# Kernel optimization log

Hardware: AMD Instinct MI355X
Metric: run time of the kernel (lower is better)

The kernel has to match this reference:

```python
import jax, jax.numpy as jnp
import numpy as np

D = 256        # n_unit
H = 2          # n_head
FF = 256       # n_hid
WIN = 99       # N-1 in source: row i attends to cols [i-99, i]
NEG = -1e30    # additive mask value (-inf in torch)
LN_EPS = 1e-5


def _layer_norm(x, w, b):
    mu = jnp.mean(x, axis=-1, keepdims=True)
    var = jnp.mean((x - mu) ** 2, axis=-1, keepdims=True)
    return (x - mu) * jax.lax.rsqrt(var + LN_EPS) * w + b


def _pos_encoding(S, d):
    pos = jnp.arange(S, dtype=jnp.float32)[:, None]                      # [S,1]
    div = jnp.exp(jnp.arange(0, d, 2, dtype=jnp.float32) * (-np.log(10000.0) / d))
    ang = pos * div                                                      # [S,d/2]
    return jnp.stack([jnp.sin(ang), jnp.cos(ang)], axis=-1).reshape(S, d)


def _band_mask(S):
    i = jnp.arange(S)[:, None]
    j = jnp.arange(S)[None, :]
    allowed = (j <= i) & (j >= i - WIN)
    return jnp.where(allowed, 0.0, NEG).astype(jnp.float32)             # [S,S]


def setup_inputs() -> dict:
    key = jax.random.key(0)
    ks = jax.random.split(key, 24)
    B, S, IN = 8, 2000, 256
    s = 0.02
    inp = {
        "src": jax.random.normal(ks[0], (B, S, IN), jnp.float32),
        "input_lengths": jax.random.randint(ks[1], (B,), 1, S + 1).astype(jnp.int64),
        # encoder Linear(in_size, n_unit); torch Linear weight is [out,in]
        "W_enc": jax.random.normal(ks[2], (D, IN), jnp.float32) * s,
        "b_enc": jnp.zeros((D,), jnp.float32),
        # MHA packed qkv projection
        "in_proj_w": jax.random.normal(ks[3], (3 * D, D), jnp.float32) * s,
        "in_proj_b": jnp.zeros((3 * D,), jnp.float32),
        "out_proj_w": jax.random.normal(ks[4], (D, D), jnp.float32) * s,
        "out_proj_b": jnp.zeros((D,), jnp.float32),
        "ln1_w": jnp.ones((D,), jnp.float32),
        "ln1_b": jnp.zeros((D,), jnp.float32),
        # FFN
        "lin1_w": jax.random.normal(ks[5], (FF, D), jnp.float32) * s,
        "lin1_b": jnp.zeros((FF,), jnp.float32),
        "lin2_w": jax.random.normal(ks[6], (D, FF), jnp.float32) * s,
        "lin2_b": jnp.zeros((D,), jnp.float32),
        "ln2_w": jnp.ones((D,), jnp.float32),
        "ln2_b": jnp.zeros((D,), jnp.float32),
        # output head
        "fc1_w": jax.random.normal(ks[7], (D // 4, D), jnp.float32) * s,
        "fc1_b": jnp.zeros((D // 4,), jnp.float32),
        "fc2_w": jax.random.normal(ks[8], (1, D // 4), jnp.float32) * s,
        "fc2_b": jnp.zeros((1,), jnp.float32),
    }
    return inp


def reference(src, input_lengths, W_enc, b_enc, in_proj_w, in_proj_b,
              out_proj_w, out_proj_b, ln1_w, ln1_b, lin1_w, lin1_b,
              lin2_w, lin2_b, ln2_w, ln2_b, fc1_w, fc1_b, fc2_w, fc2_b):
    B, S, _ = src.shape
    hd = D // H
    # input projection + positional encoding (dropout is identity at eval)
    x = src @ W_enc.T + b_enc                                            # [B,S,D]
    x = x + _pos_encoding(S, D)[None]
    # --- TransformerEncoderLayer (post-norm, relu) with banded causal mask ---
    qkv = x @ in_proj_w.T + in_proj_b                                    # [B,S,3D]
    q, k, v = jnp.split(qkv, 3, axis=-1)
    q = q.reshape(B, S, H, hd)
    k = k.reshape(B, S, H, hd)
    v = v.reshape(B, S, H, hd)
    scores = jnp.einsum('bihd,bjhd->bhij', q, k) / np.sqrt(hd)           # [B,H,S,S]
    scores = scores + _band_mask(S)[None, None]
    attn = jax.nn.softmax(scores, axis=-1)
    ctx = jnp.einsum('bhij,bjhd->bihd', attn, v).reshape(B, S, D)
    attn_out = ctx @ out_proj_w.T + out_proj_b
    x = _layer_norm(x + attn_out, ln1_w, ln1_b)
    ff = jax.nn.relu(x @ lin1_w.T + lin1_b) @ lin2_w.T + lin2_b
    x = _layer_norm(x + ff, ln2_w, ln2_b)
    # --- output head (no activation between fc1 and fc2, per source) ---
    out = x @ fc1_w.T + fc1_b                                            # [B,S,D/4]
    logits = out @ fc2_w.T + fc2_b                                       # [B,S,1]
    return logits.reshape(B, -1)                                         # [B,S]
```

## Files before the change

### kernel.cpp

```cpp
#include <hip/hip_runtime.h>
#include <math.h>

#define SLEN 2000
#define BATCH 8
#define MTOK 16000
#define WIN 99
#define XPAD 264

typedef __attribute__((ext_vector_type(8))) short short8;
typedef __attribute__((ext_vector_type(4))) float floatx4;

__device__ __forceinline__ float bf2f(unsigned int h) {
  union { unsigned int u; float f; } w; w.u = h << 16; return w.f;
}
__device__ __forceinline__ unsigned short f2bf(float f) {
  union { float f; unsigned int u; } w; w.f = f;
  return (unsigned short)((w.u + 0x7fffu + ((w.u >> 16) & 1u)) >> 16);
}

__device__ __forceinline__ void cvt4(const float* __restrict__ in,
                                     unsigned short* __restrict__ out, int i) {
  float4 v = ((const float4*)in)[i];
  ushort4 o;
  o.x = f2bf(v.x); o.y = f2bf(v.y); o.z = f2bf(v.z); o.w = f2bf(v.w);
  ((ushort4*)out)[i] = o;
}

__global__ __launch_bounds__(256) void k_prep(
    const float* __restrict__ wenc,     unsigned short* __restrict__ wencb,
    const float* __restrict__ wqk,      unsigned short* __restrict__ wqkb,
    const float* __restrict__ wout,     unsigned short* __restrict__ woutb,
    const float* __restrict__ wl1,      unsigned short* __restrict__ wl1b,
    const float* __restrict__ wl2,      unsigned short* __restrict__ wl2b,
    float* __restrict__ pe,
    const float* __restrict__ fc1w, const float* __restrict__ fc1b,
    const float* __restrict__ fc2w, const float* __restrict__ fc2b,
    const float* __restrict__ ln2w, const float* __restrict__ ln2b,
    float* __restrict__ hp) {
  __shared__ float red0[4], red1[4];
  const int bx = blockIdx.x, tid = threadIdx.x;
  if (bx < 64)         { cvt4(wenc, wencb, bx * 256 + tid); }
  else if (bx < 256)   { cvt4(wqk,  wqkb,  (bx - 64) * 256 + tid); }
  else if (bx < 320)   { cvt4(wout, woutb, (bx - 256) * 256 + tid); }
  else if (bx < 384)   { cvt4(wl1,  wl1b,  (bx - 320) * 256 + tid); }
  else if (bx < 448)   { cvt4(wl2,  wl2b,  (bx - 384) * 256 + tid); }
  else if (bx < 948) {
    int i4 = (bx - 448) * 256 + tid;
    int e0 = i4 * 4;
    int s  = e0 >> 8;
    int d0 = e0 & 255;
    float dv0 = expf((float)(d0 >> 1) * -0.07195578415606394f);
    float dv1 = expf((float)((d0 >> 1) + 1) * -0.07195578415606394f);
    float a0 = (float)s * dv0, a1 = (float)s * dv1;
    ((float4*)pe)[i4] = make_float4(sinf(a0), cosf(a0), sinf(a1), cosf(a1));
  } else {
    int k = tid;
    float we = 0.f;
#pragma unroll 8
    for (int o = 0; o < 64; ++o) we += fc2w[o] * fc1w[o * 256 + k];
    float c1 = ln2w[k] * we;
    hp[k] = c1;
    float p0 = ln2b[k] * we;
    if (k < 64) p0 += fc2w[k] * fc1b[k];
    float s0 = p0, s1 = c1;
#pragma unroll
    for (int off = 32; off; off >>= 1) {
      s0 += __shfl_xor(s0, off);
      s1 += __shfl_xor(s1, off);
    }
    int wv = k >> 6;
    if ((k & 63) == 0) { red0[wv] = s0; red1[wv] = s1; }
    __syncthreads();
    if (k == 0) {
      hp[256] = red0[0] + red0[1] + red0[2] + red0[3] + fc2b[0];
      hp[257] = red1[0] + red1[1] + red1[2] + red1[3];
    }
  }
}

__global__ __launch_bounds__(512) void k_pre(
    const float* __restrict__ src,
    const unsigned short* __restrict__ wenc, const float* __restrict__ benc,
    const float* __restrict__ pe,
    const unsigned short* __restrict__ wqk, const float* __restrict__ bqk,
    unsigned short* __restrict__ xb, unsigned short* __restrict__ qkvb) {
  __shared__ __align__(16) unsigned short Xt[64 * XPAD];
  const int tid = threadIdx.x, lane = tid & 63, w = tid >> 6;
  const int m0 = blockIdx.x * 64;
  const int kq = lane >> 4, ml = lane & 15;

  {
    const int cb = w * 32;
    floatx4 acc[4][2] = {};
#pragma unroll
    for (int k8 = 0; k8 < 8; ++k8) {
      const int kt = k8 * 32;
      short8 af[4];
#pragma unroll
      for (int mt = 0; mt < 4; ++mt) {
        const float* ap = src + (size_t)(m0 + mt * 16 + ml) * 256 + kt + kq * 8;
        float4 v0 = *(const float4*)ap;
        float4 v1 = *(const float4*)(ap + 4);
        unsigned short t8[8] = {f2bf(v0.x), f2bf(v0.y), f2bf(v0.z), f2bf(v0.w),
                                f2bf(v1.x), f2bf(v1.y), f2bf(v1.z), f2bf(v1.w)};
        af[mt] = *(const short8*)t8;
      }
#pragma unroll
      for (int nt = 0; nt < 2; ++nt) {
        short8 bf = *(const short8*)(wenc + (size_t)(cb + nt * 16 + ml) * 256 + kt + kq * 8);
#pragma unroll
        for (int mt = 0; mt < 4; ++mt)
          acc[mt][nt] = __builtin_amdgcn_mfma_f32_16x16x32_bf16(af[mt], bf, acc[mt][nt], 0, 0, 0);
      }
    }
#pragma unroll
    for (int mt = 0; mt < 4; ++mt)
#pragma unroll
      for (int nt = 0; nt < 2; ++nt)
#pragma unroll
        for (int r = 0; r < 4; ++r) {
          int lrow = mt * 16 + kq * 4 + r;
          int col  = cb + nt * 16 + ml;
          float v = acc[mt][nt][r] + benc[col]
                  + pe[(size_t)((m0 + lrow) % SLEN) * 256 + col];
          unsigned short hv = f2bf(v);
          Xt[lrow * XPAD + col] = hv;
          xb[(size_t)(m0 + lrow) * 256 + col] = hv;
        }
  }
  __syncthreads();

  {
    const int cb = w * 96;
    floatx4 acc[4][6] = {};
#pragma unroll
    for (int k8 = 0; k8 < 8; ++k8) {
      const int kt = k8 * 32;
      short8 af[4];
#pragma unroll
      for (int mt = 0; mt < 4; ++mt)
        af[mt] = *(const short8*)&Xt[(mt * 16 + ml) * XPAD + kt + kq * 8];
#pragma unroll
      for (int nt = 0; nt < 6; ++nt) {
        short8 bf = *(const short8*)(wqk + (size_t)(cb + nt * 16 + ml) * 256 + kt + kq * 8);
#pragma unroll
        for (int mt = 0; mt < 4; ++mt)
          acc[mt][nt] = __builtin_amdgcn_mfma_f32_16x16x32_bf16(af[mt], bf, acc[mt][nt], 0, 0, 0);
      }
    }
#pragma unroll
    for (int mt = 0; mt < 4; ++mt)
#pragma unroll
      for (int nt = 0; nt < 6; ++nt)
#pragma unroll
        for (int r = 0; r < 4; ++r) {
          int row = m0 + mt * 16 + kq * 4 + r;
          int cg  = cb + nt * 16 + ml;
          qkvb[(size_t)row * 768 + cg] = f2bf(acc[mt][nt][r] + bqk[cg]);
        }
  }
}

#define KPAD 136
#define VPAD 184
#define PPAD 132
#define UNION 176

__global__ __launch_bounds__(256) void k_attn_mfma(const unsigned short* __restrict__ qkv,
                                                   unsigned short* __restrict__ ctx) {
  __shared__ __align__(16) unsigned short KV[UNION * KPAD];
  __shared__ __align__(16) unsigned short Ps[4][16 * PPAD];
  const int tid  = threadIdx.x;
  const int lane = tid & 63;
  const int w    = tid >> 6;
  const int i0   = blockIdx.x * 64;
  const int b    = blockIdx.y;
  const int h    = blockIdx.z;
  const int jmin_u = i0 - WIN;
  const float scale = 0.08838834764831845f;

  const int qrow = i0 + w * 16 + (lane & 15);
  const unsigned short* qptr =
      qkv + (size_t)(b * SLEN + min(qrow, SLEN - 1)) * 768 + h * 128 + (lane >> 4) * 8;
  short8 qf[4];
#pragma unroll
  for (int kc = 0; kc < 4; ++kc) qf[kc] = *(const short8*)(qptr + kc * 32);

  for (int it = 0; it < 11; ++it) {
    int idx = it * 256 + tid;
    int row = idx >> 4;
    int c8  = idx & 15;
    int j = jmin_u + row;
    uint4 v = make_uint4(0u, 0u, 0u, 0u);
    if (j >= 0 && j < SLEN)
      v = *(const uint4*)(qkv + (size_t)(b * SLEN + j) * 768 + 256 + h * 128 + c8 * 8);
    *(uint4*)&KV[row * KPAD + c8 * 8] = v;
  }
  __syncthreads();

  const int koff = w * 16;
  floatx4 sc[8] = {};
#pragma unroll
  for (int kt = 0; kt < 8; ++kt) {
#pragma unroll
    for (int kc = 0; kc < 4; ++kc) {
      short8 kf = *(const short8*)&KV[(koff + kt * 16 + (lane & 15)) * KPAD
                                      + kc * 32 + (lane >> 4) * 8];
      sc[kt] = __builtin_amdgcn_mfma_f32_16x16x32_bf16(qf[kc], kf, sc[kt], 0, 0, 0);
    }
  }

  const int qme = i0 + w * 16 + (lane >> 4) * 4;
  const int jme = jmin_u + koff + (lane & 15);
  float mx[4] = {-1e30f, -1e30f, -1e30f, -1e30f};
#pragma unroll
  for (int kt = 0; kt < 8; ++kt) {
#pragma unroll
    for (int r = 0; r < 4; ++r) {
      int j = jme + kt * 16, q = qme + r;
      bool ok = (j >= 0) && (j >= q - WIN) && (j <= q);
      float s = ok ? sc[kt][r] : -1e30f;
      sc[kt][r] = s;
      mx[r] = fmaxf(mx[r], s);
    }
  }
#pragma unroll
  for (int r = 0; r < 4; ++r)
#pragma unroll
    for (int off = 8; off; off >>= 1) mx[r] = fmaxf(mx[r], __shfl_xor(mx[r], off, 16));

  float sum[4] = {0.f, 0.f, 0.f, 0.f};
#pragma unroll
  for (int kt = 0; kt < 8; ++kt)
#pragma unroll
    for (int r = 0; r < 4; ++r) {
      float e = __expf((sc[kt][r] - mx[r]) * scale);
      sc[kt][r] = e;
      sum[r] += e;
    }
#pragma unroll
  for (int r = 0; r < 4; ++r)
#pragma unroll
    for (int off = 8; off; off >>= 1) sum[r] += __shfl_xor(sum[r], off, 16);
  float rinv[4];
#pragma unroll
  for (int r = 0; r < 4; ++r) rinv[r] = 1.f / sum[r];

  unsigned short* pw = &Ps[w][0];
#pragma unroll
  for (int kt = 0; kt < 8; ++kt)
#pragma unroll
    for (int r = 0; r < 4; ++r)
      pw[((lane >> 4) * 4 + r) * PPAD + kt * 16 + (lane & 15)] = f2bf(sc[kt][r]);
  __syncthreads();

  for (int it = 0; it < 12; ++it) {
    int idx = it * 256 + tid;
    int grp = idx >> 6;
    int key = (grp >> 4) * 64 + (idx & 63);
    int c8  = grp & 15;
    if (key < UNION) {
      int j = jmin_u + key;
      uint4 v = make_uint4(0u, 0u, 0u, 0u);
      if (j >= 0 && j < SLEN)
        v = *(const uint4*)(qkv + (size_t)(b * SLEN + j) * 768 + 512 + h * 128 + c8 * 8);
      unsigned short e[8];
      *(uint4*)e = v;
      int d0 = c8 * 8;
#pragma unroll
      for (int i = 0; i < 8; ++i) KV[(d0 + i) * VPAD + key] = e[i];
    }
  }
  __syncthreads();

  floatx4 ov[8] = {};
#pragma unroll
  for (int kc = 0; kc < 4; ++kc) {
    short8 pf = *(const short8*)&pw[(lane & 15) * PPAD + kc * 32 + (lane >> 4) * 8];
#pragma unroll
    for (int dt = 0; dt < 8; ++dt) {
      short8 vf = *(const short8*)&KV[(dt * 16 + (lane & 15)) * VPAD
                                      + koff + kc * 32 + (lane >> 4) * 8];
      ov[dt] = __builtin_amdgcn_mfma_f32_16x16x32_bf16(pf, vf, ov[dt], 0, 0, 0);
    }
  }

#pragma unroll
  for (int dt = 0; dt < 8; ++dt)
#pragma unroll
    for (int r = 0; r < 4; ++r) {
      int q = qme + r;
      if (q < SLEN)
        ctx[(size_t)(b * SLEN + q) * 256 + h * 128 + dt * 16 + (lane & 15)] =
            f2bf(ov[dt][r] * rinv[r]);
    }
}

__global__ __launch_bounds__(512) void k_post(
    const unsigned short* __restrict__ ctx,
    const unsigned short* __restrict__ wout, const float* __restrict__ bout,
    const unsigned short* __restrict__ xb,
    const float* __restrict__ ln1w, const float* __restrict__ ln1b,
    const unsigned short* __restrict__ w1, const float* __restrict__ b1,
    const unsigned short* __restrict__ w2, const float* __restrict__ b2,
    const float* __restrict__ hp, float* __restrict__ out) {
  __shared__ __align__(16) unsigned short X1[64 * XPAD];
  __shared__ float lnred[8][64][3];
  __shared__ float lnstat[64][2];
  __shared__ float lnp[512];
  __shared__ float c1s[256];
  const int tid = threadIdx.x, lane = tid & 63, w = tid >> 6;
  const int m0 = blockIdx.x * 64;
  const int kq = lane >> 4, ml = lane & 15;
  const int cb = w * 32;

  if (tid < 256) {
    lnp[tid] = ln1w[tid];
    lnp[256 + tid] = ln1b[tid];
    c1s[tid] = hp[tid];
  }
  const float c0h = hp[256], sc1 = hp[257];

  floatx4 acc[4][2] = {};
#pragma unroll
  for (int k8 = 0; k8 < 8; ++k8) {
    const int kt = k8 * 32;
    short8 af[4];
#pragma unroll
    for (int mt = 0; mt < 4; ++mt)
      af[mt] = *(const short8*)(ctx + (size_t)(m0 + mt * 16 + ml) * 256 + kt + kq * 8);
#pragma unroll
    for (int nt = 0; nt < 2; ++nt) {
      short8 bf = *(const short8*)(wout + (size_t)(cb + nt * 16 + ml) * 256 + kt + kq * 8);
#pragma unroll
      for (int mt = 0; mt < 4; ++mt)
        acc[mt][nt] = __builtin_amdgcn_mfma_f32_16x16x32_bf16(af[mt], bf, acc[mt][nt], 0, 0, 0);
    }
  }
  float s_[4][4], q_[4][4];
#pragma unroll
  for (int mt = 0; mt < 4; ++mt)
#pragma unroll
    for (int r = 0; r < 4; ++r) { s_[mt][r] = 0.f; q_[mt][r] = 0.f; }
#pragma unroll
  for (int mt = 0; mt < 4; ++mt)
#pragma unroll
    for (int nt = 0; nt < 2; ++nt)
#pragma unroll
      for (int r = 0; r < 4; ++r) {
        int lrow = mt * 16 + kq * 4 + r;
        int col  = cb + nt * 16 + ml;
        float v = acc[mt][nt][r] + bout[col]
                + bf2f(xb[(size_t)(m0 + lrow) * 256 + col]);
        acc[mt][nt][r] = v;
        s_[mt][r] += v;
        q_[mt][r] += v * v;
      }
#pragma unroll
  for (int mt = 0; mt < 4; ++mt)
#pragma unroll
    for (int r = 0; r < 4; ++r) {
#pragma unroll
      for (int off = 8; off; off >>= 1) {
        s_[mt][r] += __shfl_xor(s_[mt][r], off, 16);
        q_[mt][r] += __shfl_xor(q_[mt][r], off, 16);
      }
      if (ml == 0) {
        int lrow = mt * 16 + kq * 4 + r;
        lnred[w][lrow][0] = s_[mt][r];
        lnred[w][lrow][1] = q_[mt][r];
      }
    }
  __syncthreads();
  if (tid < 64) {
    float s = 0.f, q = 0.f;
#pragma unroll
    for (int i = 0; i < 8; ++i) { s += lnred[i][tid][0]; q += lnred[i][tid][1]; }
    float mu  = s * (1.f / 256.f);
    float var = q * (1.f / 256.f) - mu * mu;
    lnstat[tid][0] = mu;
    lnstat[tid][1] = rsqrtf(var + 1e-5f);
  }
  __syncthreads();
  floatx4 x1sav[4][2];
#pragma unroll
  for (int mt = 0; mt < 4; ++mt)
#pragma unroll
    for (int r = 0; r < 4; ++r) {
      int lrow = mt * 16 + kq * 4 + r;
      float mu = lnstat[lrow][0], rr = lnstat[lrow][1];
#pragma unroll
      for (int nt = 0; nt < 2; ++nt) {
        int col = cb + nt * 16 + ml;
        float x1 = (acc[mt][nt][r] - mu) * rr * lnp[col] + lnp[256 + col];
        x1sav[mt][nt][r] = x1;
        X1[lrow * XPAD + col] = f2bf(x1);
      }
    }
  __syncthreads();

#pragma unroll
  for (int mt = 0; mt < 4; ++mt)
#pragma unroll
    for (int nt = 0; nt < 2; ++nt) acc[mt][nt] = (floatx4){0.f, 0.f, 0.f, 0.f};
#pragma unroll
  for (int k8 = 0; k8 < 8; ++k8) {
    const int kt = k8 * 32;
    short8 af[4];
#pragma unroll
    for (int mt = 0; mt < 4; ++mt)
      af[mt] = *(const short8*)&X1[(mt * 16 + ml) * XPAD + kt + kq * 8];
#pragma unroll
    for (int nt = 0; nt < 2; ++nt) {
      short8 bf = *(const short8*)(w1 + (size_t)(cb + nt * 16 + ml) * 256 + kt + kq * 8);
#pragma unroll
      for (int mt = 0; mt < 4; ++mt)
        acc[mt][nt] = __builtin_amdgcn_mfma_f32_16x16x32_bf16(af[mt], bf, acc[mt][nt], 0, 0, 0);
    }
  }
  __syncthreads();
#pragma unroll
  for (int mt = 0; mt < 4; ++mt)
#pragma unroll
    for (int nt = 0; nt < 2; ++nt)
#pragma unroll
      for (int r = 0; r < 4; ++r) {
        int lrow = mt * 16 + kq * 4 + r;
        int col  = cb + nt * 16 + ml;
        X1[lrow * XPAD + col] = f2bf(fmaxf(acc[mt][nt][r] + b1[col], 0.f));
      }
  __syncthreads();

#pragma unroll
  for (int mt = 0; mt < 4; ++mt)
#pragma unroll
    for (int nt = 0; nt < 2; ++nt) acc[mt][nt] = (floatx4){0.f, 0.f, 0.f, 0.f};
#pragma unroll
  for (int k8 = 0; k8 < 8; ++k8) {
    const int kt = k8 * 32;
    short8 af[4];
#pragma unroll
    for (int mt = 0; mt < 4; ++mt)
      af[mt] = *(const short8*)&X1[(mt * 16 + ml) * XPAD + kt + kq * 8];
#pragma unroll
    for (int nt = 0; nt < 2; ++nt) {
      short8 bf = *(const short8*)(w2 + (size_t)(cb + nt * 16 + ml) * 256 + kt + kq * 8);
#pragma unroll
      for (int mt = 0; mt < 4; ++mt)
        acc[mt][nt] = __builtin_amdgcn_mfma_f32_16x16x32_bf16(af[mt], bf, acc[mt][nt], 0, 0, 0);
    }
  }
  float ss[4][4], qq[4][4], dd[4][4];
#pragma unroll
  for (int mt = 0; mt < 4; ++mt)
#pragma unroll
    for (int r = 0; r < 4; ++r) { ss[mt][r] = 0.f; qq[mt][r] = 0.f; dd[mt][r] = 0.f; }
#pragma unroll
  for (int mt = 0; mt < 4; ++mt)
#pragma unroll
    for (int nt = 0; nt < 2; ++nt)
#pragma unroll
      for (int r = 0; r < 4; ++r) {
        int col = cb + nt * 16 + ml;
        float v = acc[mt][nt][r] + b2[col] + x1sav[mt][nt][r];
        ss[mt][r] += v;
        qq[mt][r] += v * v;
        dd[mt][r] += v * c1s[col];
      }
#pragma unroll
  for (int mt = 0; mt < 4; ++mt)
#pragma unroll
    for (int r = 0; r < 4; ++r) {
#pragma unroll
      for (int off = 8; off; off >>= 1) {
        ss[mt][r] += __shfl_xor(ss[mt][r], off, 16);
        qq[mt][r] += __shfl_xor(qq[mt][r], off, 16);
        dd[mt][r] += __shfl_xor(dd[mt][r], off, 16);
      }
      if (ml == 0) {
        int lrow = mt * 16 + kq * 4 + r;
        lnred[w][lrow][0] = ss[mt][r];
        lnred[w][lrow][1] = qq[mt][r];
        lnred[w][lrow][2] = dd[mt][r];
      }
    }
  __syncthreads();
  if (tid < 64) {
    float s = 0.f, q = 0.f, d = 0.f;
#pragma unroll
    for (int i = 0; i < 8; ++i) {
      s += lnred[i][tid][0];
      q += lnred[i][tid][1];
      d += lnred[i][tid][2];
    }
    float mu  = s * (1.f / 256.f);
    float var = q * (1.f / 256.f) - mu * mu;
    float rr  = rsqrtf(var + 1e-5f);
    out[m0 + tid] = rr * (d - mu * sc1) + c0h;
  }
}

extern "C" void kernel_launch(void* const* d_in, const int* in_sizes, int n_in,
                              void* d_out, int out_size, void* d_ws, size_t ws_size,
                              hipStream_t stream) {
  const float* src        = (const float*)d_in[0];
  const float* W_enc      = (const float*)d_in[2];
  const float* b_enc      = (const float*)d_in[3];
  const float* in_proj_w  = (const float*)d_in[4];
  const float* in_proj_b  = (const float*)d_in[5];
  const float* out_proj_w = (const float*)d_in[6];
  const float* out_proj_b = (const float*)d_in[7];
  const float* ln1_w      = (const float*)d_in[8];
  const float* ln1_b      = (const float*)d_in[9];
  const float* lin1_w     = (const float*)d_in[10];
  const float* lin1_b     = (const float*)d_in[11];
  const float* lin2_w     = (const float*)d_in[12];
  const float* lin2_b     = (const float*)d_in[13];
  const float* ln2_w      = (const float*)d_in[14];
  const float* ln2_b      = (const float*)d_in[15];
  const float* fc1_w      = (const float*)d_in[16];
  const float* fc1_b      = (const float*)d_in[17];
  const float* fc2_w      = (const float*)d_in[18];
  const float* fc2_b      = (const float*)d_in[19];

  char* p = (char*)d_ws;
  float* pe            = (float*)p;           p += (size_t)SLEN * 256 * 4;
  float* hp            = (float*)p;           p += 2048;
  unsigned short* xb   = (unsigned short*)p;  p += (size_t)MTOK * 256 * 2;
  unsigned short* qkvb = (unsigned short*)p;  p += (size_t)MTOK * 768 * 2;
  unsigned short* ctxb = (unsigned short*)p;  p += (size_t)MTOK * 256 * 2;
  unsigned short* wencb= (unsigned short*)p;  p += 256 * 256 * 2;
  unsigned short* wqkb = (unsigned short*)p;  p += 768 * 256 * 2;
  unsigned short* woutb= (unsigned short*)p;  p += 256 * 256 * 2;
  unsigned short* wl1b = (unsigned short*)p;  p += 256 * 256 * 2;
  unsigned short* wl2b = (unsigned short*)p;  p += 256 * 256 * 2;

  k_prep<<<949, 256, 0, stream>>>(W_enc, wencb, in_proj_w, wqkb,
                                  out_proj_w, woutb, lin1_w, wl1b, lin2_w, wl2b,
                                  pe, fc1_w, fc1_b, fc2_w, fc2_b, ln2_w, ln2_b, hp);
  k_pre<<<MTOK / 64, 512, 0, stream>>>(src, wencb, b_enc, pe, wqkb, in_proj_b, xb, qkvb);
  k_attn_mfma<<<dim3((SLEN + 63) / 64, BATCH, 2), 256, 0, stream>>>(qkvb, ctxb);
  k_post<<<MTOK / 64, 512, 0, stream>>>(ctxb, woutb, out_proj_b, xb, ln1_w, ln1_b,
                                        wl1b, lin1_b, wl2b, lin2_b, hp, (float*)d_out);
}
```

Before: 188.8 us.

## Fuse attention with post-projection/FFN, drop prep kernel and compute posenc inline

Removes the separate weight-conversion/positional-encoding prep kernel. Weights are now converted fp32->bf16 on the fly inside the GEMM loops, and positional encoding is computed inline with fast sin. Attention for both heads is merged with the out-projection, LN, FFN and output head into a single kernel, so the ctx buffer round-trip through global memory disappears. Blocks change from 512 to 256 threads. The trade-offs are redundant weight conversion per block, fewer attention blocks (the head dimension moves into the loop), and heavier shared-memory use, which may lower occupancy.

New measurement: 235.1 us. 24.5% more time.

```diff
diff --git a/kernel.cpp b/kernel.cpp
--- a/kernel.cpp
+++ b/kernel.cpp
@@ -17,146 +17,92 @@
   union { float f; unsigned int u; } w; w.f = f;
   return (unsigned short)((w.u + 0x7fffu + ((w.u >> 16) & 1u)) >> 16);
 }
-
-__device__ __forceinline__ void cvt4(const float* __restrict__ in,
-                                     unsigned short* __restrict__ out, int i) {
-  float4 v = ((const float4*)in)[i];
-  ushort4 o;
-  o.x = f2bf(v.x); o.y = f2bf(v.y); o.z = f2bf(v.z); o.w = f2bf(v.w);
-  ((ushort4*)out)[i] = o;
-}
-
-__global__ __launch_bounds__(256) void k_prep(
-    const float* __restrict__ wenc,     unsigned short* __restrict__ wencb,
-    const float* __restrict__ wqk,      unsigned short* __restrict__ wqkb,
-    const float* __restrict__ wout,     unsigned short* __restrict__ woutb,
-    const float* __restrict__ wl1,      unsigned short* __restrict__ wl1b,
-    const float* __restrict__ wl2,      unsigned short* __restrict__ wl2b,
-    float* __restrict__ pe,
-    const float* __restrict__ fc1w, const float* __restrict__ fc1b,
-    const float* __restrict__ fc2w, const float* __restrict__ fc2b,
-    const float* __restrict__ ln2w, const float* __restrict__ ln2b,
-    float* __restrict__ hp) {
-  __shared__ float red0[4], red1[4];
-  const int bx = blockIdx.x, tid = threadIdx.x;
-  if (bx < 64)         { cvt4(wenc, wencb, bx * 256 + tid); }
-  else if (bx < 256)   { cvt4(wqk,  wqkb,  (bx - 64) * 256 + tid); }
-  else if (bx < 320)   { cvt4(wout, woutb, (bx - 256) * 256 + tid); }
-  else if (bx < 384)   { cvt4(wl1,  wl1b,  (bx - 320) * 256 + tid); }
-  else if (bx < 448)   { cvt4(wl2,  wl2b,  (bx - 384) * 256 + tid); }
-  else if (bx < 948) {
-    int i4 = (bx - 448) * 256 + tid;
-    int e0 = i4 * 4;
-    int s  = e0 >> 8;
-    int d0 = e0 & 255;
-    float dv0 = expf((float)(d0 >> 1) * -0.07195578415606394f);
-    float dv1 = expf((float)((d0 >> 1) + 1) * -0.07195578415606394f);
-    float a0 = (float)s * dv0, a1 = (float)s * dv1;
-    ((float4*)pe)[i4] = make_float4(sinf(a0), cosf(a0), sinf(a1), cosf(a1));
-  } else {
-    int k = tid;
-    float we = 0.f;
-#pragma unroll 8
-    for (int o = 0; o < 64; ++o) we += fc2w[o] * fc1w[o * 256 + k];
-    float c1 = ln2w[k] * we;
-    hp[k] = c1;
-    float p0 = ln2b[k] * we;
-    if (k < 64) p0 += fc2w[k] * fc1b[k];
-    float s0 = p0, s1 = c1;
-#pragma unroll
-    for (int off = 32; off; off >>= 1) {
-      s0 += __shfl_xor(s0, off);
-      s1 += __shfl_xor(s1, off);
-    }
-    int wv = k >> 6;
-    if ((k & 63) == 0) { red0[wv] = s0; red1[wv] = s1; }
-    __syncthreads();
-    if (k == 0) {
-      hp[256] = red0[0] + red0[1] + red0[2] + red0[3] + fc2b[0];
-      hp[257] = red1[0] + red1[1] + red1[2] + red1[3];
-    }
-  }
-}
-
-__global__ __launch_bounds__(512) void k_pre(
+__device__ __forceinline__ short8 cvt_row8(const float* __restrict__ p) {
+  float4 v0 = *(const float4*)p;
+  float4 v1 = *(const float4*)(p + 4);
+  unsigned short t8[8] = {f2bf(v0.x), f2bf(v0.y), f2bf(v0.z), f2bf(v0.w),
+                          f2bf(v1.x), f2bf(v1.y), f2bf(v1.z), f2bf(v1.w)};
+  return *(const short8*)t8;
+}
+__device__ __forceinline__ float posenc_val(int spos, int col) {
+  float p   = (float)(col >> 1);
+  float dv  = __expf(p * -0.07195578415606394f);
+  float ang = (float)spos * dv;
+  float rev = ang * 0.15915494309189535f;
+  rev -= floorf(rev);
+  if (col & 1) { rev += 0.25f; rev -= floorf(rev); }
+  return __sinf(rev * 6.283185307179586f);
+}
+
+__global__ __launch_bounds__(256) void k_pre(
     const float* __restrict__ src,
-    const unsigned short* __restrict__ wenc, const float* __restrict__ benc,
-    const float* __restrict__ pe,
-    const unsigned short* __restrict__ wqk, const float* __restrict__ bqk,
+    const float* __restrict__ wenc, const float* __restrict__ benc,
+    const float* __restrict__ wqk,  const float* __restrict__ bqk,
     unsigned short* __restrict__ xb, unsigned short* __restrict__ qkvb) {
   __shared__ __align__(16) unsigned short Xt[64 * XPAD];
   const int tid = threadIdx.x, lane = tid & 63, w = tid >> 6;
   const int m0 = blockIdx.x * 64;
   const int kq = lane >> 4, ml = lane & 15;
-
-  {
-    const int cb = w * 32;
-    floatx4 acc[4][2] = {};
+  const int wcol = w * 64;
+
+  floatx4 acc[4][4] = {};
+#pragma unroll
+  for (int k8 = 0; k8 < 8; ++k8) {
+    const int kt = k8 * 32;
+    short8 af[4];
+#pragma unroll
+    for (int mt = 0; mt < 4; ++mt)
+      af[mt] = cvt_row8(src + (size_t)(m0 + mt * 16 + ml) * 256 + kt + kq * 8);
+#pragma unroll
+    for (int nt = 0; nt < 4; ++nt) {
+      short8 bf = cvt_row8(wenc + (size_t)(wcol + nt * 16 + ml) * 256 + kt + kq * 8);
+#pragma unroll
+      for (int mt = 0; mt < 4; ++mt)
+        acc[mt][nt] = __builtin_amdgcn_mfma_f32_16x16x32_bf16(af[mt], bf, acc[mt][nt], 0, 0, 0);
+    }
+  }
+#pragma unroll
+  for (int mt = 0; mt < 4; ++mt)
+#pragma unroll
+    for (int nt = 0; nt < 4; ++nt)
+#pragma unroll
+      for (int r = 0; r < 4; ++r) {
+        int lrow = mt * 16 + kq * 4 + r;
+        int col  = wcol + nt * 16 + ml;
+        int spos = (m0 + lrow) % SLEN;
+        float v = acc[mt][nt][r] + benc[col] + posenc_val(spos, col);
+        unsigned short hv = f2bf(v);
+        Xt[lrow * XPAD + col] = hv;
+        xb[(size_t)(m0 + lrow) * 256 + col] = hv;
+      }
+  __syncthreads();
+
+  for (int p = 0; p < 3; ++p) {
+    floatx4 a2[4][4] = {};
 #pragma unroll
     for (int k8 = 0; k8 < 8; ++k8) {
       const int kt = k8 * 32;
       short8 af[4];
 #pragma unroll
-      for (int mt = 0; mt < 4; ++mt) {
-        const float* ap = src + (size_t)(m0 + mt * 16 + ml) * 256 + kt + kq * 8;
-        float4 v0 = *(const float4*)ap;
-        float4 v1 = *(const float4*)(ap + 4);
-        unsigned short t8[8] = {f2bf(v0.x), f2bf(v0.y), f2bf(v0.z), f2bf(v0.w),
-                                f2bf(v1.x), f2bf(v1.y), f2bf(v1.z), f2bf(v1.w)};
-        af[mt] = *(const short8*)t8;
-      }
-#pragma unroll
-      for (int nt = 0; nt < 2; ++nt) {
-        short8 bf = *(const short8*)(wenc + (size_t)(cb + nt * 16 + ml) * 256 + kt + kq * 8);
-#pragma unroll
-        for (int mt = 0; mt < 4; ++mt)
-          acc[mt][nt] = __builtin_amdgcn_mfma_f32_16x16x32_bf16(af[mt], bf, acc[mt][nt], 0, 0, 0);
-      }
-    }
-#pragma unroll
-    for (int mt = 0; mt < 4; ++mt)
-#pragma unroll
-      for (int nt = 0; nt < 2; ++nt)
-#pragma unroll
-        for (int r = 0; r < 4; ++r) {
-          int lrow = mt * 16 + kq * 4 + r;
-          int col  = cb + nt * 16 + ml;
-          float v = acc[mt][nt][r] + benc[col]
-                  + pe[(size_t)((m0 + lrow) % SLEN) * 256 + col];
-          unsigned short hv = f2bf(v);
-          Xt[lrow * XPAD + col] = hv;
-          xb[(size_t)(m0 + lrow) * 256 + col] = hv;
-        }
-  }
-  __syncthreads();
-
-  {
-    const int cb = w * 96;
-    floatx4 acc[4][6] = {};
-#pragma unroll
-    for (int k8 = 0; k8 < 8; ++k8) {
-      const int kt = k8 * 32;
-      short8 af[4];
-#pragma unroll
       for (int mt = 0; mt < 4; ++mt)
         af[mt] = *(const short8*)&Xt[(mt * 16 + ml) * XPAD + kt + kq * 8];
 #pragma unroll
-      for (int nt = 0; nt < 6; ++nt) {
-        short8 bf = *(const short8*)(wqk + (size_t)(cb + nt * 16 + ml) * 256 + kt + kq * 8);
+      for (int nt = 0; nt < 4; ++nt) {
+        short8 bf = cvt_row8(wqk + (size_t)(p * 256 + wcol + nt * 16 + ml) * 256 + kt + kq * 8);
 #pragma unroll
         for (int mt = 0; mt < 4; ++mt)
-          acc[mt][nt] = __builtin_amdgcn_mfma_f32_16x16x32_bf16(af[mt], bf, acc[mt][nt], 0, 0, 0);
+          a2[mt][nt] = __builtin_amdgcn_mfma_f32_16x16x32_bf16(af[mt], bf, a2[mt][nt], 0, 0, 0);
       }
     }
 #pragma unroll
     for (int mt = 0; mt < 4; ++mt)
 #pragma unroll
-      for (int nt = 0; nt < 6; ++nt)
+      for (int nt = 0; nt < 4; ++nt)
 #pragma unroll
         for (int r = 0; r < 4; ++r) {
           int row = m0 + mt * 16 + kq * 4 + r;
-          int cg  = cb + nt * 16 + ml;
-          qkvb[(size_t)row * 768 + cg] = f2bf(acc[mt][nt][r] + bqk[cg]);
+          int cg  = p * 256 + wcol + nt * 16 + ml;
+          qkvb[(size_t)row * 768 + cg] = f2bf(a2[mt][nt][r] + bqk[cg]);
         }
   }
 }
@@ -166,172 +112,188 @@
 #define PPAD 132
 #define UNION 176
 
-__global__ __launch_bounds__(256) void k_attn_mfma(const unsigned short* __restrict__ qkv,
-                                                   unsigned short* __restrict__ ctx) {
-  __shared__ __align__(16) unsigned short KV[UNION * KPAD];
-  __shared__ __align__(16) unsigned short Ps[4][16 * PPAD];
-  const int tid  = threadIdx.x;
-  const int lane = tid & 63;
-  const int w    = tid >> 6;
-  const int i0   = blockIdx.x * 64;
-  const int b    = blockIdx.y;
-  const int h    = blockIdx.z;
+__global__ __launch_bounds__(256) void k_ap(
+    const unsigned short* __restrict__ qkv,
+    const unsigned short* __restrict__ xb,
+    const float* __restrict__ wout, const float* __restrict__ bout,
+    const float* __restrict__ ln1w, const float* __restrict__ ln1b,
+    const float* __restrict__ w1,   const float* __restrict__ b1,
+    const float* __restrict__ w2,   const float* __restrict__ b2,
+    const float* __restrict__ fc1w, const float* __restrict__ fc1b,
+    const float* __restrict__ fc2w, const float* __restrict__ fc2b,
+    const float* __restrict__ ln2w, const float* __restrict__ ln2b,
+    float* __restrict__ out) {
+  __shared__ __align__(16) unsigned char smem[64768];
+  unsigned short* KV  = (unsigned short*)smem;
+  unsigned short* Ps  = (unsigned short*)(smem + 47872);
+  unsigned short* CX  = (unsigned short*)smem;
+  float* lnred  = (float*)(smem + 33792);
+  float* lnstat = (float*)(smem + 36864);
+  float* lnp    = (float*)(smem + 37376);
+  float* c1s    = (float*)(smem + 39424);
+  float* hpred  = (float*)(smem + 40448);
+  float* hpc    = (float*)(smem + 40480);
+
+  const int tid = threadIdx.x, lane = tid & 63, w = tid >> 6;
+  const int i0 = blockIdx.x * 64;
+  const int b  = blockIdx.y;
   const int jmin_u = i0 - WIN;
+  const int kq = lane >> 4, ml = lane & 15;
   const float scale = 0.08838834764831845f;
 
-  const int qrow = i0 + w * 16 + (lane & 15);
-  const unsigned short* qptr =
-      qkv + (size_t)(b * SLEN + min(qrow, SLEN - 1)) * 768 + h * 128 + (lane >> 4) * 8;
-  short8 qf[4];
-#pragma unroll
-  for (int kc = 0; kc < 4; ++kc) qf[kc] = *(const short8*)(qptr + kc * 32);
-
-  for (int it = 0; it < 11; ++it) {
-    int idx = it * 256 + tid;
-    int row = idx >> 4;
-    int c8  = idx & 15;
-    int j = jmin_u + row;
-    uint4 v = make_uint4(0u, 0u, 0u, 0u);
-    if (j >= 0 && j < SLEN)
-      v = *(const uint4*)(qkv + (size_t)(b * SLEN + j) * 768 + 256 + h * 128 + c8 * 8);
-    *(uint4*)&KV[row * KPAD + c8 * 8] = v;
-  }
-  __syncthreads();
-
-  const int koff = w * 16;
-  floatx4 sc[8] = {};
-#pragma unroll
-  for (int kt = 0; kt < 8; ++kt) {
-#pragma unroll
-    for (int kc = 0; kc < 4; ++kc) {
-      short8 kf = *(const short8*)&KV[(koff + kt * 16 + (lane & 15)) * KPAD
-                                      + kc * 32 + (lane >> 4) * 8];
-      sc[kt] = __builtin_amdgcn_mfma_f32_16x16x32_bf16(qf[kc], kf, sc[kt], 0, 0, 0);
-    }
-  }
-
-  const int qme = i0 + w * 16 + (lane >> 4) * 4;
-  const int jme = jmin_u + koff + (lane & 15);
-  float mx[4] = {-1e30f, -1e30f, -1e30f, -1e30f};
-#pragma unroll
-  for (int kt = 0; kt < 8; ++kt) {
-#pragma unroll
-    for (int r = 0; r < 4; ++r) {
-      int j = jme + kt * 16, q = qme + r;
-      bool ok = (j >= 0) && (j >= q - WIN) && (j <= q);
-      float s = ok ? sc[kt][r] : -1e30f;
-      sc[kt][r] = s;
-      mx[r] = fmaxf(mx[r], s);
-    }
-  }
-#pragma unroll
-  for (int r = 0; r < 4; ++r)
-#pragma unroll
-    for (int off = 8; off; off >>= 1) mx[r] = fmaxf(mx[r], __shfl_xor(mx[r], off, 16));
-
-  float sum[4] = {0.f, 0.f, 0.f, 0.f};
-#pragma unroll
-  for (int kt = 0; kt < 8; ++kt)
-#pragma unroll
-    for (int r = 0; r < 4; ++r) {
-      float e = __expf((sc[kt][r] - mx[r]) * scale);
-      sc[kt][r] = e;
-      sum[r] += e;
-    }
-#pragma unroll
-  for (int r = 0; r < 4; ++r)
-#pragma unroll
-    for (int off = 8; off; off >>= 1) sum[r] += __shfl_xor(sum[r], off, 16);
-  float rinv[4];
-#pragma unroll
-  for (int r = 0; r < 4; ++r) rinv[r] = 1.f / sum[r];
-
-  unsigned short* pw = &Ps[w][0];
-#pragma unroll
-  for (int kt = 0; kt < 8; ++kt)
-#pragma unroll
-    for (int r = 0; r < 4; ++r)
-      pw[((lane >> 4) * 4 + r) * PPAD + kt * 16 + (lane & 15)] = f2bf(sc[kt][r]);
-  __syncthreads();
-
-  for (int it = 0; it < 12; ++it) {
-    int idx = it * 256 + tid;
-    int grp = idx >> 6;
-    int key = (grp >> 4) * 64 + (idx & 63);
-    int c8  = grp & 15;
-    if (key < UNION) {
-      int j = jmin_u + key;
+  floatx4 ovh[2][8];
+  for (int h = 0; h < 2; ++h) {
+    if (h) __syncthreads();
+
+    const int qrow = i0 + w * 16 + ml;
+    const unsigned short* qptr =
+        qkv + (size_t)(b * SLEN + min(qrow, SLEN - 1)) * 768 + h * 128 + kq * 8;
+    short8 qf[4];
+#pragma unroll
+    for (int kc = 0; kc < 4; ++kc) qf[kc] = *(const short8*)(qptr + kc * 32);
+
+    for (int it = 0; it < 11; ++it) {
+      int idx = it * 256 + tid;
+      int row = idx >> 4;
+      int c8  = idx & 15;
+      int j = jmin_u + row;
       uint4 v = make_uint4(0u, 0u, 0u, 0u);
       if (j >= 0 && j < SLEN)
-        v = *(const uint4*)(qkv + (size_t)(b * SLEN + j) * 768 + 512 + h * 128 + c8 * 8);
-      unsigned short e[8];
-      *(uint4*)e = v;
-      int d0 = c8 * 8;
-#pragma unroll
-      for (int i = 0; i < 8; ++i) KV[(d0 + i) * VPAD + key] = e[i];
-    }
-  }
-  __syncthreads();
-
-  floatx4 ov[8] = {};
-#pragma unroll
-  for (int kc = 0; kc < 4; ++kc) {
-    short8 pf = *(const short8*)&pw[(lane & 15) * PPAD + kc * 32 + (lane >> 4) * 8];
-#pragma unroll
-    for (int dt = 0; dt < 8; ++dt) {
-      short8 vf = *(const short8*)&KV[(dt * 16 + (lane & 15)) * VPAD
-                                      + koff + kc * 32 + (lane >> 4) * 8];
-      ov[dt] = __builtin_amdgcn_mfma_f32_16x16x32_bf16(pf, vf, ov[dt], 0, 0, 0);
-    }
-  }
-
-#pragma unroll
-  for (int dt = 0; dt < 8; ++dt)
-#pragma unroll
-    for (int r = 0; r < 4; ++r) {
-      int q = qme + r;
-      if (q < SLEN)
-        ctx[(size_t)(b * SLEN + q) * 256 + h * 128 + dt * 16 + (lane & 15)] =
-            f2bf(ov[dt][r] * rinv[r]);
-    }
-}
-
-__global__ __launch_bounds__(512) void k_post(
-    const unsigned short* __restrict__ ctx,
-    const unsigned short* __restrict__ wout, const float* __restrict__ bout,
-    const unsigned short* __restrict__ xb,
-    const float* __restrict__ ln1w, const float* __restrict__ ln1b,
-    const unsigned short* __restrict__ w1, const float* __restrict__ b1,
-    const unsigned short* __restrict__ w2, const float* __restrict__ b2,
-    const float* __restrict__ hp, float* __restrict__ out) {
-  __shared__ __align__(16) unsigned short X1[64 * XPAD];
-  __shared__ float lnred[8][64][3];
-  __shared__ float lnstat[64][2];
-  __shared__ float lnp[512];
-  __shared__ float c1s[256];
-  const int tid = threadIdx.x, lane = tid & 63, w = tid >> 6;
-  const int m0 = blockIdx.x * 64;
-  const int kq = lane >> 4, ml = lane & 15;
-  const int cb = w * 32;
-
-  if (tid < 256) {
-    lnp[tid] = ln1w[tid];
-    lnp[256 + tid] = ln1b[tid];
-    c1s[tid] = hp[tid];
-  }
-  const float c0h = hp[256], sc1 = hp[257];
-
-  floatx4 acc[4][2] = {};
+        v = *(const uint4*)(qkv + (size_t)(b * SLEN + j) * 768 + 256 + h * 128 + c8 * 8);
+      *(uint4*)&KV[row * KPAD + c8 * 8] = v;
+    }
+    __syncthreads();
+
+    const int koff = w * 16;
+    floatx4 sc[8] = {};
+#pragma unroll
+    for (int kt = 0; kt < 8; ++kt) {
+#pragma unroll
+      for (int kc = 0; kc < 4; ++kc) {
+        short8 kf = *(const short8*)&KV[(koff + kt * 16 + ml) * KPAD + kc * 32 + kq * 8];
+        sc[kt] = __builtin_amdgcn_mfma_f32_16x16x32_bf16(qf[kc], kf, sc[kt], 0, 0, 0);
+      }
+    }
+
+    const int qme = i0 + w * 16 + kq * 4;
+    const int jme = jmin_u + koff + ml;
+    float mx[4] = {-1e30f, -1e30f, -1e30f, -1e30f};
+#pragma unroll
+    for (int kt = 0; kt < 8; ++kt)
+#pragma unroll
+      for (int r = 0; r < 4; ++r) {
+        int j = jme + kt * 16, q = qme + r;
+        bool ok = (j >= 0) && (j >= q - WIN) && (j <= q);
+        float s = ok ? sc[kt][r] : -1e30f;
+        sc[kt][r] = s;
+        mx[r] = fmaxf(mx[r], s);
+      }
+#pragma unroll
+    for (int r = 0; r < 4; ++r)
+#pragma unroll
+      for (int off = 8; off; off >>= 1) mx[r] = fmaxf(mx[r], __shfl_xor(mx[r], off, 16));
+
+    float sum[4] = {0.f, 0.f, 0.f, 0.f};
+#pragma unroll
+    for (int kt = 0; kt < 8; ++kt)
+#pragma unroll
+      for (int r = 0; r < 4; ++r) {
+        float e = __expf((sc[kt][r] - mx[r]) * scale);
+        sc[kt][r] = e;
+        sum[r] += e;
+      }
+#pragma unroll
+    for (int r = 0; r < 4; ++r)
+#pragma unroll
+      for (int off = 8; off; off >>= 1) sum[r] += __shfl_xor(sum[r], off, 16);
+    float rinv[4];
+#pragma unroll
+    for (int r = 0; r < 4; ++r) rinv[r] = 1.f / sum[r];
+
+    unsigned short* pw = Ps + w * (16 * PPAD);
+#pragma unroll
+    for (int kt = 0; kt < 8; ++kt)
+#pragma unroll
+      for (int r = 0; r < 4; ++r)
+        pw[(kq * 4 + r) * PPAD + kt * 16 + ml] = f2bf(sc[kt][r]);
+    __syncthreads();
+
+    for (int it = 0; it < 12; ++it) {
+      int idx = it * 256 + tid;
+      int grp = idx >> 6;
+      int key = (grp >> 4) * 64 + (idx & 63);
+      int c8  = grp & 15;
+      if (key < UNION) {
+        int j = jmin_u + key;
+        uint4 v = make_uint4(0u, 0u, 0u, 0u);
+        if (j >= 0 && j < SLEN)
+          v = *(const uint4*)(qkv + (size_t)(b * SLEN + j) * 768 + 512 + h * 128 + c8 * 8);
+        unsigned short e[8];
+        *(uint4*)e = v;
+        int d0 = c8 * 8;
+#pragma unroll
+        for (int i = 0; i < 8; ++i) KV[(d0 + i) * VPAD + key] = e[i];
+      }
+    }
+    __syncthreads();
+
+#pragma unroll
+    for (int dt = 0; dt < 8; ++dt) ovh[h][dt] = (floatx4){0.f, 0.f, 0.f, 0.f};
+#pragma unroll
+    for (int kc = 0; kc < 4; ++kc) {
+      short8 pf = *(const short8*)&pw[ml * PPAD + kc * 32 + kq * 8];
+#pragma unroll
+      for (int dt = 0; dt < 8; ++dt) {
+        short8 vf = *(const short8*)&KV[(dt * 16 + ml) * VPAD + koff + kc * 32 + kq * 8];
+        ovh[h][dt] = __builtin_amdgcn_mfma_f32_16x16x32_bf16(pf, vf, ovh[h][dt], 0, 0, 0);
+      }
+    }
+#pragma unroll
+    for (int dt = 0; dt < 8; ++dt)
+#pragma unroll
+      for (int r = 0; r < 4; ++r) ovh[h][dt][r] *= rinv[r];
+  }
+  __syncthreads();
+
+#pragma unroll
+  for (int h = 0; h < 2; ++h)
+#pragma unroll
+    for (int dt = 0; dt < 8; ++dt)
+#pragma unroll
+      for (int r = 0; r < 4; ++r)
+        CX[(w * 16 + kq * 4 + r) * XPAD + h * 128 + dt * 16 + ml] = f2bf(ovh[h][dt][r]);
+  lnp[tid] = ln1w[tid];
+  lnp[256 + tid] = ln1b[tid];
+  {
+    float we = 0.f;
+#pragma unroll 8
+    for (int o = 0; o < 64; ++o) we += fc2w[o] * fc1w[o * 256 + tid];
+    float c1 = ln2w[tid] * we;
+    c1s[tid] = c1;
+    float p0 = ln2b[tid] * we;
+    if (tid < 64) p0 += fc2w[tid] * fc1b[tid];
+    float s0 = p0, s1 = c1;
+#pragma unroll
+    for (int off = 32; off; off >>= 1) {
+      s0 += __shfl_xor(s0, off);
+      s1 += __shfl_xor(s1, off);
+    }
+    if (lane == 0) { hpred[w * 2] = s0; hpred[w * 2 + 1] = s1; }
+  }
+  __syncthreads();
+
+  const int wcol = w * 64;
+  floatx4 acc[4][4] = {};
 #pragma unroll
   for (int k8 = 0; k8 < 8; ++k8) {
     const int kt = k8 * 32;
     short8 af[4];
 #pragma unroll
     for (int mt = 0; mt < 4; ++mt)
-      af[mt] = *(const short8*)(ctx + (size_t)(m0 + mt * 16 + ml) * 256 + kt + kq * 8);
-#pragma unroll
-    for (int nt = 0; nt < 2; ++nt) {
-      short8 bf = *(const short8*)(wout + (size_t)(cb + nt * 16 + ml) * 256 + kt + kq * 8);
+      af[mt] = *(const short8*)&CX[(mt * 16 + ml) * XPAD + kt + kq * 8];
+#pragma unroll
+    for (int nt = 0; nt < 4; ++nt) {
+      short8 bf = cvt_row8(wout + (size_t)(wcol + nt * 16 + ml) * 256 + kt + kq * 8);
 #pragma unroll
       for (int mt = 0; mt < 4; ++mt)
         acc[mt][nt] = __builtin_amdgcn_mfma_f32_16x16x32_bf16(af[mt], bf, acc[mt][nt], 0, 0, 0);
@@ -345,13 +307,14 @@
 #pragma unroll
   for (int mt = 0; mt < 4; ++mt)
 #pragma unroll
-    for (int nt = 0; nt < 2; ++nt)
+    for (int nt = 0; nt < 4; ++nt)
 #pragma unroll
       for (int r = 0; r < 4; ++r) {
         int lrow = mt * 16 + kq * 4 + r;
-        int col  = cb + nt * 16 + ml;
+        int rm   = min(i0 + lrow, SLEN - 1);
+        int col  = wcol + nt * 16 + ml;
         float v = acc[mt][nt][r] + bout[col]
-                + bf2f(xb[(size_t)(m0 + lrow) * 256 + col]);
+                + bf2f(xb[(size_t)(b * SLEN + rm) * 256 + col]);
         acc[mt][nt][r] = v;
         s_[mt][r] += v;
         q_[mt][r] += v * v;
@@ -367,52 +330,59 @@
       }
       if (ml == 0) {
         int lrow = mt * 16 + kq * 4 + r;
-        lnred[w][lrow][0] = s_[mt][r];
-        lnred[w][lrow][1] = q_[mt][r];
+        lnred[(w * 64 + lrow) * 3 + 0] = s_[mt][r];
+        lnred[(w * 64 + lrow) * 3 + 1] = q_[mt][r];
       }
     }
   __syncthreads();
   if (tid < 64) {
     float s = 0.f, q = 0.f;
 #pragma unroll
-    for (int i = 0; i < 8; ++i) { s += lnred[i][tid][0]; q += lnred[i][tid][1]; }
+    for (int i = 0; i < 4; ++i) {
+      s += lnred[(i * 64 + tid) * 3 + 0];
+      q += lnred[(i * 64 + tid) * 3 + 1];
+    }
     float mu  = s * (1.f / 256.f);
     float var = q * (1.f / 256.f) - mu * mu;
-    lnstat[tid][0] = mu;
-    lnstat[tid][1] = rsqrtf(var + 1e-5f);
-  }
-  __syncthreads();
-  floatx4 x1sav[4][2];
+    lnstat[tid * 2 + 0] = mu;
+    lnstat[tid * 2 + 1] = rsqrtf(var + 1e-5f);
+  }
+  if (tid == 64) {
+    hpc[0] = hpred[0] + hpred[2] + hpred[4] + hpred[6] + fc2b[0];
+    hpc[1] = hpred[1] + hpred[3] + hpred[5] + hpred[7];
+  }
+  __syncthreads();
+  floatx4 x1sav[4][4];
 #pragma unroll
   for (int mt = 0; mt < 4; ++mt)
 #pragma unroll
     for (int r = 0; r < 4; ++r) {
       int lrow = mt * 16 + kq * 4 + r;
-      float mu = lnstat[lrow][0], rr = lnstat[lrow][1];
-#pragma unroll
-      for (int nt = 0; nt < 2; ++nt) {
-        int col = cb + nt * 16 + ml;
+      float mu = lnstat[lrow * 2], rr = lnstat[lrow * 2 + 1];
+#pragma unroll
+      for (int nt = 0; nt < 4; ++nt) {
+        int col = wcol + nt * 16 + ml;
         float x1 = (acc[mt][nt][r] - mu) * rr * lnp[col] + lnp[256 + col];
         x1sav[mt][nt][r] = x1;
-        X1[lrow * XPAD + col] = f2bf(x1);
-      }
-    }
-  __syncthreads();
-
-#pragma unroll
-  for (int mt = 0; mt < 4; ++mt)
-#pragma unroll
-    for (int nt = 0; nt < 2; ++nt) acc[mt][nt] = (floatx4){0.f, 0.f, 0.f, 0.f};
+        CX[lrow * XPAD + col] = f2bf(x1);
+      }
+    }
+  __syncthreads();
+
+#pragma unroll
+  for (int mt = 0; mt < 4; ++mt)
+#pragma unroll
+    for (int nt = 0; nt < 4; ++nt) acc[mt][nt] = (floatx4){0.f, 0.f, 0.f, 0.f};
 #pragma unroll
   for (int k8 = 0; k8 < 8; ++k8) {
     const int kt = k8 * 32;
     short8 af[4];
 #pragma unroll
     for (int mt = 0; mt < 4; ++mt)
-      af[mt] = *(const short8*)&X1[(mt * 16 + ml) * XPAD + kt + kq * 8];
-#pragma unroll
-    for (int nt = 0; nt < 2; ++nt) {
-      short8 bf = *(const short8*)(w1 + (size_t)(cb + nt * 16 + ml) * 256 + kt + kq * 8);
+      af[mt] = *(const short8*)&CX[(mt * 16 + ml) * XPAD + kt + kq * 8];
+#pragma unroll
+    for (int nt = 0; nt < 4; ++nt) {
+      short8 bf = cvt_row8(w1 + (size_t)(wcol + nt * 16 + ml) * 256 + kt + kq * 8);
 #pragma unroll
       for (int mt = 0; mt < 4; ++mt)
         acc[mt][nt] = __builtin_amdgcn_mfma_f32_16x16x32_bf16(af[mt], bf, acc[mt][nt], 0, 0, 0);
@@ -422,29 +392,29 @@
 #pragma unroll
   for (int mt = 0; mt < 4; ++mt)
 #pragma unroll
-    for (int nt = 0; nt < 2; ++nt)
+    for (int nt = 0; nt < 4; ++nt)
 #pragma unroll
       for (int r = 0; r < 4; ++r) {
         int lrow = mt * 16 + kq * 4 + r;
-        int col  = cb + nt * 16 + ml;
-        X1[lrow * XPAD + col] = f2bf(fmaxf(acc[mt][nt][r] + b1[col], 0.f));
-      }
-  __syncthreads();
-
-#pragma unroll
-  for (int mt = 0; mt < 4; ++mt)
-#pragma unroll
-    for (int nt = 0; nt < 2; ++nt) acc[mt][nt] = (floatx4){0.f, 0.f, 0.f, 0.f};
+        int col  = wcol + nt * 16 + ml;
+        CX[lrow * XPAD + col] = f2bf(fmaxf(acc[mt][nt][r] + b1[col], 0.f));
+      }
+  __syncthreads();
+
+#pragma unroll
+  for (int mt = 0; mt < 4; ++mt)
+#pragma unroll
+    for (int nt = 0; nt < 4; ++nt) acc[mt][nt] = (floatx4){0.f, 0.f, 0.f, 0.f};
 #pragma unroll
   for (int k8 = 0; k8 < 8; ++k8) {
     const int kt = k8 * 32;
     short8 af[4];
 #pragma unroll
     for (int mt = 0; mt < 4; ++mt)
-      af[mt] = *(const short8*)&X1[(mt * 16 + ml) * XPAD + kt + kq * 8];
-#pragma unroll
-    for (int nt = 0; nt < 2; ++nt) {
-      short8 bf = *(const short8*)(w2 + (size_t)(cb + nt * 16 + ml) * 256 + kt + kq * 8);
+      af[mt] = *(const short8*)&CX[(mt * 16 + ml) * XPAD + kt + kq * 8];
+#pragma unroll
+    for (int nt = 0; nt < 4; ++nt) {
+      short8 bf = cvt_row8(w2 + (size_t)(wcol + nt * 16 + ml) * 256 + kt + kq * 8);
 #pragma unroll
       for (int mt = 0; mt < 4; ++mt)
         acc[mt][nt] = __builtin_amdgcn_mfma_f32_16x16x32_bf16(af[mt], bf, acc[mt][nt], 0, 0, 0);
@@ -458,10 +428,10 @@
 #pragma unroll
   for (int mt = 0; mt < 4; ++mt)
 #pragma unroll
-    for (int nt = 0; nt < 2; ++nt)
+    for (int nt = 0; nt < 4; ++nt)
 #pragma unroll
       for (int r = 0; r < 4; ++r) {
-        int col = cb + nt * 16 + ml;
+        int col = wcol + nt * 16 + ml;
         float v = acc[mt][nt][r] + b2[col] + x1sav[mt][nt][r];
         ss[mt][r] += v;
         qq[mt][r] += v * v;
@@ -479,24 +449,24 @@
       }
       if (ml == 0) {
         int lrow = mt * 16 + kq * 4 + r;
-        lnred[w][lrow][0] = ss[mt][r];
-        lnred[w][lrow][1] = qq[mt][r];
-        lnred[w][lrow][2] = dd[mt][r];
-      }
-    }
-  __syncthreads();
-  if (tid < 64) {
+        lnred[(w * 64 + lrow) * 3 + 0] = ss[mt][r];
+        lnred[(w * 64 + lrow) * 3 + 1] = qq[mt][r];
+        lnred[(w * 64 + lrow) * 3 + 2] = dd[mt][r];
+      }
+    }
+  __syncthreads();
+  if (tid < 64 && i0 + tid < SLEN) {
     float s = 0.f, q = 0.f, d = 0.f;
 #pragma unroll
-    for (int i = 0; i < 8; ++i) {
-      s += lnred[i][tid][0];
-      q += lnred[i][tid][1];
-      d += lnred[i][tid][2];
+    for (int i = 0; i < 4; ++i) {
+      s += lnred[(i * 64 + tid) * 3 + 0];
+      q += lnred[(i * 64 + tid) * 3 + 1];
+      d += lnred[(i * 64 + tid) * 3 + 2];
     }
     float mu  = s * (1.f / 256.f);
     float var = q * (1.f / 256.f) - mu * mu;
     float rr  = rsqrtf(var + 1e-5f);
-    out[m0 + tid] = rr * (d - mu * sc1) + c0h;
+    out[(size_t)b * SLEN + i0 + tid] = rr * (d - mu * hpc[1]) + hpc[0];
   }
 }
 
@@ -524,22 +494,12 @@
   const float* fc2_b      = (const float*)d_in[19];
 
   char* p = (char*)d_ws;
-  float* pe            = (float*)p;           p += (size_t)SLEN * 256 * 4;
-  float* hp            = (float*)p;           p += 2048;
   unsigned short* xb   = (unsigned short*)p;  p += (size_t)MTOK * 256 * 2;
   unsigned short* qkvb = (unsigned short*)p;  p += (size_t)MTOK * 768 * 2;
-  unsigned short* ctxb = (unsigned short*)p;  p += (size_t)MTOK * 256 * 2;
-  unsigned short* wencb= (unsigned short*)p;  p += 256 * 256 * 2;
-  unsigned short* wqkb = (unsigned short*)p;  p += 768 * 256 * 2;
-  unsigned short* woutb= (unsigned short*)p;  p += 256 * 256 * 2;
-  unsigned short* wl1b = (unsigned short*)p;  p += 256 * 256 * 2;
-  unsigned short* wl2b = (unsigned short*)p;  p += 256 * 256 * 2;
-
-  k_prep<<<949, 256, 0, stream>>>(W_enc, wencb, in_proj_w, wqkb,
-                                  out_proj_w, woutb, lin1_w, wl1b, lin2_w, wl2b,
-                                  pe, fc1_w, fc1_b, fc2_w, fc2_b, ln2_w, ln2_b, hp);
-  k_pre<<<MTOK / 64, 512, 0, stream>>>(src, wencb, b_enc, pe, wqkb, in_proj_b, xb, qkvb);
-  k_attn_mfma<<<dim3((SLEN + 63) / 64, BATCH, 2), 256, 0, stream>>>(qkvb, ctxb);
-  k_post<<<MTOK / 64, 512, 0, stream>>>(ctxb, woutb, out_proj_b, xb, ln1_w, ln1_b,
-                                        wl1b, lin1_b, wl2b, lin2_b, hp, (float*)d_out);
-}
+
+  k_pre<<<MTOK / 64, 256, 0, stream>>>(src, W_enc, b_enc, in_proj_w, in_proj_b, xb, qkvb);
+  k_ap<<<dim3((SLEN + 63) / 64, BATCH), 256, 0, stream>>>(
+      qkvb, xb, out_proj_w, out_proj_b, ln1_w, ln1_b,
+      lin1_w, lin1_b, lin2_w, lin2_b,
+      fc1_w, fc1_b, fc2_w, fc2_b, ln2_w, ln2_b, (float*)d_out);
+}
```
